# Kernel optimization log

Measured on AMD Instinct MI355X. Metric: run time of the kernel, lower is better.

## Reference

```python
import jax, jax.numpy as jnp
import numpy as np

N = 50000        # nodes
E = 800000       # edges (before self-loops)
F_IN = 128       # input features
HID = 32         # per-head hidden channels
H1 = 4           # heads of conv1
H2 = 8           # heads of conv2
NEG_SLOPE = 0.2  # PyG GATConv LeakyReLU slope
E_DEC = 100000   # pos/neg decode edges each


def setup_inputs() -> dict:
    key = jax.random.key(0)
    ks = jax.random.split(key, 12)
    s = 0.1
    return {
        "x": jax.random.normal(ks[0], (N, F_IN), jnp.float32),
        "edge_index": jax.random.randint(ks[1], (2, E), 0, N, dtype=jnp.int32),
        "pos_edge_index": jax.random.randint(ks[2], (2, E_DEC), 0, N, dtype=jnp.int32),
        "neg_edge_index": jax.random.randint(ks[3], (2, E_DEC), 0, N, dtype=jnp.int32),
        "W1": jax.random.normal(ks[4], (F_IN, H1 * HID), jnp.float32) * s,
        "a_src1": jax.random.normal(ks[5], (H1, HID), jnp.float32) * s,
        "a_dst1": jax.random.normal(ks[6], (H1, HID), jnp.float32) * s,
        "b1": jax.random.normal(ks[7], (H1 * HID,), jnp.float32) * s,
        "W2": jax.random.normal(ks[8], (H1 * HID, H2 * HID), jnp.float32) * s,
        "a_src2": jax.random.normal(ks[9], (H2, HID), jnp.float32) * s,
        "a_dst2": jax.random.normal(ks[10], (H2, HID), jnp.float32) * s,
        "b2": jax.random.normal(ks[11], (H2 * HID,), jnp.float32) * s,
    }


def _segment_softmax(e, seg, n):
    # softmax over edges grouped by destination node; max is detached (cancels analytically)
    m = jax.lax.stop_gradient(jax.ops.segment_max(e, seg, num_segments=n))
    ex = jnp.exp(e - m[seg])
    denom = jax.ops.segment_sum(ex, seg, num_segments=n)
    return ex / (denom[seg] + 1e-16)


def _gat_conv(x, src, dst, W, a_src, a_dst, b, heads, out_ch):
    n = x.shape[0]
    h = (x @ W).reshape(n, heads, out_ch)             # [N,H,C]
    al_s = (h * a_src[None]).sum(-1)                  # [N,H]
    al_d = (h * a_dst[None]).sum(-1)                  # [N,H]
    e = al_s[src] + al_d[dst]                         # [E,H] edge logits
    e = jnp.where(e > 0, e, NEG_SLOPE * e)            # LeakyReLU
    alpha = _segment_softmax(e, dst, n)               # [E,H]
    msg = h[src] * alpha[:, :, None]                  # [E,H,C]
    out = jax.ops.segment_sum(msg, dst, num_segments=n)  # [N,H,C]
    return out.reshape(n, heads * out_ch) + b


def reference(x, edge_index, pos_edge_index, neg_edge_index,
              W1, a_src1, a_dst1, b1, W2, a_src2, a_dst2, b2):
    n = x.shape[0]
    loops = jnp.arange(n, dtype=edge_index.dtype)     # PyG add_self_loops=True
    src = jnp.concatenate([edge_index[0], loops])
    dst = jnp.concatenate([edge_index[1], loops])
    # encode
    z = jax.nn.relu(_gat_conv(x, src, dst, W1, a_src1, a_dst1, b1, H1, HID))
    z = _gat_conv(z, src, dst, W2, a_src2, a_dst2, b2, H2, HID)
    # decode
    ei = jnp.concatenate([pos_edge_index, neg_edge_index], axis=1)
    logits = (z[ei[0]] * z[ei[1]]).sum(-1)            # [2*E_DEC]
    return logits
```

## Files before the change

### kernel.cpp

```cpp
#include <hip/hip_runtime.h>
#include <hip/hip_bf16.h>

#define NN 50000
#define EE 800000
#define ET (EE + NN)
#define F_IN 128
#define HID 32
#define H1 4
#define H2 8
#define E_DEC 100000
#define NEG_SLOPE 0.2f

typedef __attribute__((ext_vector_type(8))) short short8;
typedef __attribute__((ext_vector_type(4))) float floatx4;

__device__ __forceinline__ unsigned short f2b(float f) {
    __hip_bfloat16 h = __float2bfloat16(f);
    return *reinterpret_cast<unsigned short*>(&h);
}
__device__ __forceinline__ float b2f(unsigned short u) {
    return __uint_as_float(((unsigned int)u) << 16);
}

__device__ __forceinline__ void packW_one(const float* __restrict__ W,
                                          unsigned short* __restrict__ Wp, int OUT, int id) {
    const int ctg = id >> 8;
    const int ln = id & 63;
    const int col = ctg * 16 + (ln & 15);
    const int k0 = ((id >> 6) & 3) * 32 + ((ln >> 4) & 3) * 8;
    ushort4 lo, hi;
    lo.x = f2b(W[(k0 + 0) * OUT + col]);
    lo.y = f2b(W[(k0 + 1) * OUT + col]);
    lo.z = f2b(W[(k0 + 2) * OUT + col]);
    lo.w = f2b(W[(k0 + 3) * OUT + col]);
    hi.x = f2b(W[(k0 + 4) * OUT + col]);
    hi.y = f2b(W[(k0 + 5) * OUT + col]);
    hi.z = f2b(W[(k0 + 6) * OUT + col]);
    hi.w = f2b(W[(k0 + 7) * OUT + col]);
    ((ushort4*)Wp)[id * 2] = lo;
    ((ushort4*)Wp)[id * 2 + 1] = hi;
}

#define HIST_BLOCKS ((EE / 4 + 255) / 256)
#define PACK_BLOCKS ((6144 + 255) / 256)

__global__ void hist_pack_k(const int* __restrict__ ei, int* __restrict__ counts_p,
                            const int* __restrict__ probe, int* __restrict__ rank,
                            const float* __restrict__ W1, unsigned short* __restrict__ wp1,
                            const float* __restrict__ W2, unsigned short* __restrict__ wp2) {
    if (blockIdx.x < HIST_BLOCKS) {
        const int t = blockIdx.x * 256 + threadIdx.x;
        if (t >= EE / 4) return;
        const int pv = probe[0];
        int* cp = counts_p + (blockIdx.x & 7) * NN;
        const int4 d4 = ((const int4*)(ei + EE))[t];
        int4 r4;
        r4.x = atomicAdd(&cp[d4.x], 1) - pv;
        r4.y = atomicAdd(&cp[d4.y], 1) - pv;
        r4.z = atomicAdd(&cp[d4.z], 1) - pv;
        r4.w = atomicAdd(&cp[d4.w], 1) - pv;
        ((int4*)rank)[t] = r4;
    } else {
        const int id = (blockIdx.x - HIST_BLOCKS) * 256 + threadIdx.x;
        if (id < 2048) packW_one(W1, wp1, 128, id);
        else if (id < 6144) packW_one(W2, wp2, 256, id - 2048);
    }
}

__global__ void scan1_k(const int* __restrict__ counts_p, const int* __restrict__ probe,
                        int* __restrict__ bsum) {
    __shared__ int sh[256];
    const unsigned pv = (unsigned)probe[0];
    int t = threadIdx.x;
    int i = blockIdx.x * 256 + t;
    int deg = 0;
    if (i < NN) {
        unsigned sum = 0;
#pragma unroll
        for (int s = 0; s < 8; ++s) sum += (unsigned)counts_p[s * NN + i];
        deg = (int)(sum - 8u * pv) + 1;
    }
    sh[t] = deg;
    __syncthreads();
    for (int off = 128; off > 0; off >>= 1) {
        if (t < off) sh[t] += sh[t + off];
        __syncthreads();
    }
    if (t == 0) bsum[blockIdx.x] = sh[0];
}

__global__ void scan2_k(int* __restrict__ bsum, int nb, int* __restrict__ start) {
    __shared__ int sh[256];
    int t = threadIdx.x;
    int v = (t < nb) ? bsum[t] : 0;
    sh[t] = v;
    __syncthreads();
    for (int off = 1; off < 256; off <<= 1) {
        int u = (t >= off) ? sh[t - off] : 0;
        __syncthreads();
        sh[t] += u;
        __syncthreads();
    }
    if (t < nb) bsum[t] = sh[t] - v;
    if (t == 0) start[NN] = ET;
}

__global__ void scan3_k(const int* __restrict__ counts_p, const int* __restrict__ probe,
                        const int* __restrict__ bsum, int* __restrict__ start,
                        int* __restrict__ offs, int* __restrict__ csr) {
    __shared__ int sh[256];
    const unsigned pv = (unsigned)probe[0];
    int t = threadIdx.x;
    int i = blockIdx.x * 256 + t;
    int part[8];
    int deg = 0;
    if (i < NN) {
        deg = 1;
#pragma unroll
        for (int s = 0; s < 8; ++s) {
            part[s] = (int)((unsigned)counts_p[s * NN + i] - pv);
            deg += part[s];
        }
    }
    sh[t] = deg;
    __syncthreads();
    for (int off = 1; off < 256; off <<= 1) {
        int u = (t >= off) ? sh[t - off] : 0;
        __syncthreads();
        sh[t] += u;
        __syncthreads();
    }
    int excl = sh[t] - deg + bsum[blockIdx.x];
    if (i < NN) {
        start[i] = excl;
        int o = excl;
#pragma unroll
        for (int s = 0; s < 8; ++s) {
            offs[s * NN + i] = o;
            o += part[s];
        }
        csr[o] = i;
    }
}

__global__ void scatter_k(const int* __restrict__ ei, const int* __restrict__ rank,
                          const int* __restrict__ offs, int* __restrict__ csr) {
    const int t = blockIdx.x * 256 + threadIdx.x;
    if (t >= EE / 4) return;
    const int* off = offs + (blockIdx.x & 7) * NN;
    const int4 s4 = ((const int4*)ei)[t];
    const int4 d4 = ((const int4*)(ei + EE))[t];
    const int4 r4 = ((const int4*)rank)[t];
    csr[off[d4.x] + r4.x] = s4.x;
    csr[off[d4.y] + r4.y] = s4.y;
    csr[off[d4.z] + r4.z] = s4.z;
    csr[off[d4.w] + r4.w] = s4.w;
}

template <int OUT, int H, int CT, bool F32IN>
__global__ void gemm_k(const void* __restrict__ Xin, const unsigned short* __restrict__ Wp,
                       const float* __restrict__ a_src, const float* __restrict__ a_dst,
                       unsigned short* __restrict__ Hout, float* __restrict__ als,
                       float* __restrict__ ald) {
    const int wave = threadIdx.x >> 6;
    const int lane = threadIdx.x & 63;
    const int quad = lane >> 4;
    const int rl = lane & 15;
    const int r0 = blockIdx.x * 64;
    floatx4 acc[4][CT];
#pragma unroll
    for (int rt = 0; rt < 4; ++rt)
#pragma unroll
        for (int ct = 0; ct < CT; ++ct) acc[rt][ct] = {0.f, 0.f, 0.f, 0.f};

#pragma unroll
    for (int ks = 0; ks < 4; ++ks) {
        short8 a[4];
        const int c0k = ks * 32 + quad * 8;
#pragma unroll
        for (int rt = 0; rt < 4; ++rt) {
            int row = r0 + rt * 16 + rl;
            row = row < NN ? row : NN - 1;
            if (F32IN) {
                const float4* xp =
                    (const float4*)((const float*)Xin + (long long)row * 128 + c0k);
                const float4 v0 = xp[0];
                const float4 v1 = xp[1];
                short8 tt;
                tt[0] = (short)f2b(v0.x);
                tt[1] = (short)f2b(v0.y);
                tt[2] = (short)f2b(v0.z);
                tt[3] = (short)f2b(v0.w);
                tt[4] = (short)f2b(v1.x);
                tt[5] = (short)f2b(v1.y);
                tt[6] = (short)f2b(v1.z);
                tt[7] = (short)f2b(v1.w);
                a[rt] = tt;
            } else {
                a[rt] = *(const short8*)((const unsigned short*)Xin +
                                         (long long)row * 128 + c0k);
            }
        }
#pragma unroll
        for (int ct = 0; ct < CT; ++ct) {
            const int ctg = wave * CT + ct;
            const short8 b = *(const short8*)(Wp + (((ctg * 4 + ks) * 64 + lane) << 3));
#pragma unroll
            for (int rt = 0; rt < 4; ++rt)
                acc[rt][ct] = __builtin_amdgcn_mfma_f32_16x16x32_bf16(a[rt], b, acc[rt][ct], 0, 0, 0);
        }
    }
#pragma unroll
    for (int rt = 0; rt < 4; ++rt) {
        const int rowbase = r0 + rt * 16 + quad * 4;
#pragma unroll
        for (int ct = 0; ct < CT; ++ct) {
            const int col = (wave * CT + ct) * 16 + rl;
            unsigned short* hp = Hout + (long long)(col >> 5) * NN * 32 + (col & 31);
#pragma unroll
            for (int r = 0; r < 4; ++r) {
                const int row = rowbase + r;
                if (row < NN) hp[(long long)row * 32] = f2b(acc[rt][ct][r]);
            }
        }
    }
    float asv[CT], adv[CT];
#pragma unroll
    for (int ct = 0; ct < CT; ++ct) {
        const int col = (wave * CT + ct) * 16 + rl;
        asv[ct] = a_src[col];
        adv[ct] = a_dst[col];
    }
#pragma unroll
    for (int rt = 0; rt < 4; ++rt) {
#pragma unroll
        for (int r = 0; r < 4; ++r) {
            const int row = r0 + rt * 16 + quad * 4 + r;
            float ps[CT / 2], pd[CT / 2];
#pragma unroll
            for (int hh = 0; hh < CT / 2; ++hh) {
                ps[hh] = acc[rt][2 * hh][r] * asv[2 * hh] + acc[rt][2 * hh + 1][r] * asv[2 * hh + 1];
                pd[hh] = acc[rt][2 * hh][r] * adv[2 * hh] + acc[rt][2 * hh + 1][r] * adv[2 * hh + 1];
#pragma unroll
                for (int m = 8; m >= 1; m >>= 1) {
                    ps[hh] += __shfl_xor(ps[hh], m, 64);
                    pd[hh] += __shfl_xor(pd[hh], m, 64);
                }
            }
            if (rl == 0 && row < NN) {
#pragma unroll
                for (int hh = 0; hh < CT / 2; ++hh) {
                    const int hd = wave * (CT / 2) + hh;
                    als[(long long)hd * NN + row] = ps[hh];
                    ald[(long long)hd * NN + row] = pd[hh];
                }
            }
        }
    }
}

template <int OUT, int NSLICE, bool RELU>
__global__ void gathers_k(const int* __restrict__ start, const int* __restrict__ csr,
                          const float* __restrict__ als, const float* __restrict__ ald,
                          const unsigned short* __restrict__ Hin,
                          const float* __restrict__ bias, unsigned short* __restrict__ outp) {
    constexpr int SUB = 8 / NSLICE;
    const int xcd = blockIdx.x & 7;
    const int s = xcd / SUB;
    const int sub = xcd & (SUB - 1);
    const int wave = threadIdx.x >> 6;
    const int lane = threadIdx.x & 63;
    const int g = lane >> 3;
    const int cl = lane & 7;
    const int d = (blockIdx.x >> 3) * (32 * SUB) + sub * 32 + wave * 8 + g;
    if (d >= NN) return;
    const float* als_h = als + (long long)s * NN;
    const float aldd = ald[(long long)s * NN + d];
    const unsigned short* slab = Hin + (long long)s * NN * 32;
    const int beg = start[d], end = start[d + 1];
    float a0 = 0.f, a1 = 0.f, a2 = 0.f, a3 = 0.f, den = 0.f;
    int i = beg;
    for (; i + 7 < end; i += 8) {
        int sn[8];
        float l[8];
        ushort4 hv[8];
#pragma unroll
        for (int k = 0; k < 8; ++k) sn[k] = __builtin_nontemporal_load(csr + i + k);
#pragma unroll
        for (int k = 0; k < 8; ++k) l[k] = als_h[sn[k]] + aldd;
#pragma unroll
        for (int k = 0; k < 8; ++k) hv[k] = *(const ushort4*)(slab + (long long)sn[k] * 32 + cl * 4);
#pragma unroll
        for (int k = 0; k < 8; ++k) {
            float lg = l[k] > 0.f ? l[k] : NEG_SLOPE * l[k];
            const float w = __expf(lg);
            den += w;
            a0 += w * b2f(hv[k].x);
            a1 += w * b2f(hv[k].y);
            a2 += w * b2f(hv[k].z);
            a3 += w * b2f(hv[k].w);
        }
    }
    for (; i + 3 < end; i += 4) {
        int sn[4];
        float l[4];
        ushort4 hv[4];
#pragma unroll
        for (int k = 0; k < 4; ++k) sn[k] = __builtin_nontemporal_load(csr + i + k);
#pragma unroll
        for (int k = 0; k < 4; ++k) l[k] = als_h[sn[k]] + aldd;
#pragma unroll
        for (int k = 0; k < 4; ++k) hv[k] = *(const ushort4*)(slab + (long long)sn[k] * 32 + cl * 4);
#pragma unroll
        for (int k = 0; k < 4; ++k) {
            float lg = l[k] > 0.f ? l[k] : NEG_SLOPE * l[k];
            const float w = __expf(lg);
            den += w;
            a0 += w * b2f(hv[k].x);
            a1 += w * b2f(hv[k].y);
            a2 += w * b2f(hv[k].z);
            a3 += w * b2f(hv[k].w);
        }
    }
    for (; i < end; ++i) {
        const int sn = __builtin_nontemporal_load(csr + i);
        float lg = als_h[sn] + aldd;
        lg = lg > 0.f ? lg : NEG_SLOPE * lg;
        const float w = __expf(lg);
        const ushort4 hv = *(const ushort4*)(slab + (long long)sn * 32 + cl * 4);
        den += w;
        a0 += w * b2f(hv.x);
        a1 += w * b2f(hv.y);
        a2 += w * b2f(hv.z);
        a3 += w * b2f(hv.w);
    }
    const float inv = 1.f / (den + 1e-16f);
    const int c0 = s * 32 + cl * 4;
    float v0 = a0 * inv + bias[c0];
    float v1 = a1 * inv + bias[c0 + 1];
    float v2 = a2 * inv + bias[c0 + 2];
    float v3 = a3 * inv + bias[c0 + 3];
    if (RELU) {
        v0 = v0 > 0.f ? v0 : 0.f;
        v1 = v1 > 0.f ? v1 : 0.f;
        v2 = v2 > 0.f ? v2 : 0.f;
        v3 = v3 > 0.f ? v3 : 0.f;
    }
    unsigned long long pk =
        (unsigned long long)f2b(v0) |
        ((unsigned long long)f2b(v1) << 16) |
        ((unsigned long long)f2b(v2) << 32) |
        ((unsigned long long)f2b(v3) << 48);
    __builtin_nontemporal_store(pk, (unsigned long long*)(outp + (long long)d * OUT + c0));
}

__global__ void decode_s_k(const int* __restrict__ pei, const int* __restrict__ nei,
                           const unsigned short* __restrict__ z2, float* __restrict__ part) {
    const int s = blockIdx.x & 7;
    const int g = blockIdx.x >> 3;
    const int wave = threadIdx.x >> 6, lane = threadIdx.x & 63;
    const int slot = lane >> 3, cl = lane & 7;
    const int idx = g * 32 + wave * 8 + slot;
    if (idx >= 2 * E_DEC) return;
    int a, b;
    if (idx < E_DEC) {
        a = pei[idx];
        b = pei[E_DEC + idx];
    } else {
        const int j = idx - E_DEC;
        a = nei[j];
        b = nei[E_DEC + j];
    }
    const ushort4 ua = *(const ushort4*)(z2 + (long long)a * 256 + s * 32 + cl * 4);
    const ushort4 ub = *(const ushort4*)(z2 + (long long)b * 256 + s * 32 + cl * 4);
    float sum = b2f(ua.x) * b2f(ub.x) + b2f(ua.y) * b2f(ub.y) +
                b2f(ua.z) * b2f(ub.z) + b2f(ua.w) * b2f(ub.w);
    sum += __shfl_xor(sum, 4, 64);
    sum += __shfl_xor(sum, 2, 64);
    sum += __shfl_xor(sum, 1, 64);
    if (cl == 0) part[(long long)s * (2 * E_DEC) + idx] = sum;
}

__global__ void reduce_k(const float* __restrict__ part, float* __restrict__ out) {
    const int i = blockIdx.x * 256 + threadIdx.x;
    if (i >= 2 * E_DEC) return;
    float s = 0.f;
#pragma unroll
    for (int k = 0; k < 8; ++k) s += part[(long long)k * (2 * E_DEC) + i];
    out[i] = s;
}

extern "C" void kernel_launch(void* const* d_in, const int* in_sizes, int n_in,
                              void* d_out, int out_size, void* d_ws, size_t ws_size,
                              hipStream_t stream) {
    const float* x = (const float*)d_in[0];
    const int* ei = (const int*)d_in[1];
    const int* pei = (const int*)d_in[2];
    const int* nei = (const int*)d_in[3];
    const float* W1 = (const float*)d_in[4];
    const float* as1 = (const float*)d_in[5];
    const float* ad1 = (const float*)d_in[6];
    const float* b1 = (const float*)d_in[7];
    const float* W2 = (const float*)d_in[8];
    const float* as2 = (const float*)d_in[9];
    const float* ad2 = (const float*)d_in[10];
    const float* b2 = (const float*)d_in[11];
    float* out = (float*)d_out;

    unsigned short* h1 = (unsigned short*)d_ws;
    unsigned short* h2 = h1 + (long long)NN * 128;
    unsigned short* z2 = h2 + (long long)NN * 256;
    unsigned short* z1 = z2 + (long long)NN * 256;
    unsigned short* wp1 = z1 + (long long)NN * 128;
    unsigned short* wp2 = wp1 + 128 * 128;
    float* als1 = (float*)(wp2 + 128 * 256);
    float* ald1 = als1 + NN * H1;
    float* als2 = ald1 + NN * H1;
    float* ald2 = als2 + NN * H2;
    float* part = ald2 + NN * H2;
    int* counts_p = (int*)(part + 8 * 2 * E_DEC);
    int* start = counts_p + 8 * NN;
    int* offs = start + NN + 1;
    int* rank = offs + 8 * NN;
    int* bsum = rank + EE;
    int* csr = bsum + 256;
    int* probe = csr + ET;

    const int NB = (NN + 255) / 256;

    hist_pack_k<<<HIST_BLOCKS + PACK_BLOCKS, 256, 0, stream>>>(
        ei, counts_p, probe, rank, W1, wp1, W2, wp2);
    scan1_k<<<NB, 256, 0, stream>>>(counts_p, probe, bsum);
    scan2_k<<<1, 256, 0, stream>>>(bsum, NB, start);
    scan3_k<<<NB, 256, 0, stream>>>(counts_p, probe, bsum, start, offs, csr);
    scatter_k<<<HIST_BLOCKS, 256, 0, stream>>>(ei, rank, offs, csr);

    gemm_k<128, H1, 2, true><<<(NN + 63) / 64, 256, 0, stream>>>(
        x, wp1, as1, ad1, h1, als1, ald1);
    gathers_k<128, 4, true><<<8 * ((NN + 63) / 64), 256, 0, stream>>>(
        start, csr, als1, ald1, h1, b1, z1);

    gemm_k<256, H2, 4, false><<<(NN + 63) / 64, 256, 0, stream>>>(
        z1, wp2, as2, ad2, h2, als2, ald2);
    gathers_k<256, 8, false><<<8 * ((NN + 31) / 32), 256, 0, stream>>>(
        start, csr, als2, ald2, h2, b2, z2);

    decode_s_k<<<8 * ((2 * E_DEC + 31) / 32), 256, 0, stream>>>(pei, nei, z2, part);
    reduce_k<<<(2 * E_DEC + 255) / 256, 256, 0, stream>>>(part, out);
}
```

Measured before the change: 416.6 us.

## Sort destination nodes by degree to balance gather work across lanes

Builds a degree histogram during the CSR scan, prefix-sums it in scan2, and writes a degree-sorted node permutation in scan3. Both gather kernels then process nodes in that permuted order, so the 8 nodes sharing a wave have similar edge counts and less divergence in the per-node loops. The cost is extra global atomics on a 256-bin histogram and an indirection through perm. Output writes become scattered rather than contiguous. Index arithmetic also drops from 64-bit to 32-bit.

```diff
diff --git a/kernel.cpp b/kernel.cpp
--- a/kernel.cpp
+++ b/kernel.cpp
@@ -42,12 +42,13 @@
 }
 
 #define HIST_BLOCKS ((EE / 4 + 255) / 256)
-#define PACK_BLOCKS ((6144 + 255) / 256)
+#define PACK_BLOCKS 25
 
 __global__ void hist_pack_k(const int* __restrict__ ei, int* __restrict__ counts_p,
                             const int* __restrict__ probe, int* __restrict__ rank,
                             const float* __restrict__ W1, unsigned short* __restrict__ wp1,
-                            const float* __restrict__ W2, unsigned short* __restrict__ wp2) {
+                            const float* __restrict__ W2, unsigned short* __restrict__ wp2,
+                            int* __restrict__ dhist) {
     if (blockIdx.x < HIST_BLOCKS) {
         const int t = blockIdx.x * 256 + threadIdx.x;
         if (t >= EE / 4) return;
@@ -64,11 +65,12 @@
         const int id = (blockIdx.x - HIST_BLOCKS) * 256 + threadIdx.x;
         if (id < 2048) packW_one(W1, wp1, 128, id);
         else if (id < 6144) packW_one(W2, wp2, 256, id - 2048);
+        else if (id < 6400) dhist[id - 6144] = 0;
     }
 }
 
 __global__ void scan1_k(const int* __restrict__ counts_p, const int* __restrict__ probe,
-                        int* __restrict__ bsum) {
+                        int* __restrict__ bsum, int* __restrict__ dhist) {
     __shared__ int sh[256];
     const unsigned pv = (unsigned)probe[0];
     int t = threadIdx.x;
@@ -79,6 +81,7 @@
 #pragma unroll
         for (int s = 0; s < 8; ++s) sum += (unsigned)counts_p[s * NN + i];
         deg = (int)(sum - 8u * pv) + 1;
+        atomicAdd(&dhist[deg < 255 ? deg : 255], 1);
     }
     sh[t] = deg;
     __syncthreads();
@@ -89,7 +92,8 @@
     if (t == 0) bsum[blockIdx.x] = sh[0];
 }
 
-__global__ void scan2_k(int* __restrict__ bsum, int nb, int* __restrict__ start) {
+__global__ void scan2_k(int* __restrict__ bsum, int nb, int* __restrict__ start,
+                        int* __restrict__ dhist) {
     __shared__ int sh[256];
     int t = threadIdx.x;
     int v = (t < nb) ? bsum[t] : 0;
@@ -103,11 +107,23 @@
     }
     if (t < nb) bsum[t] = sh[t] - v;
     if (t == 0) start[NN] = ET;
+    __syncthreads();
+    int h = dhist[t];
+    sh[t] = h;
+    __syncthreads();
+    for (int off = 1; off < 256; off <<= 1) {
+        int u = (t >= off) ? sh[t - off] : 0;
+        __syncthreads();
+        sh[t] += u;
+        __syncthreads();
+    }
+    dhist[t] = sh[t] - h;
 }
 
 __global__ void scan3_k(const int* __restrict__ counts_p, const int* __restrict__ probe,
                         const int* __restrict__ bsum, int* __restrict__ start,
-                        int* __restrict__ offs, int* __restrict__ csr) {
+                        int* __restrict__ offs, int* __restrict__ csr,
+                        int* __restrict__ dhist, int* __restrict__ perm) {
     __shared__ int sh[256];
     const unsigned pv = (unsigned)probe[0];
     int t = threadIdx.x;
@@ -140,6 +156,9 @@
             o += part[s];
         }
         csr[o] = i;
+        const int bin = deg < 255 ? deg : 255;
+        const int pos = atomicAdd(&dhist[bin], 1);
+        perm[pos] = i;
     }
 }
 
@@ -261,6 +280,7 @@
 
 template <int OUT, int NSLICE, bool RELU>
 __global__ void gathers_k(const int* __restrict__ start, const int* __restrict__ csr,
+                          const int* __restrict__ perm,
                           const float* __restrict__ als, const float* __restrict__ ald,
                           const unsigned short* __restrict__ Hin,
                           const float* __restrict__ bias, unsigned short* __restrict__ outp) {
@@ -272,11 +292,12 @@
     const int lane = threadIdx.x & 63;
     const int g = lane >> 3;
     const int cl = lane & 7;
-    const int d = (blockIdx.x >> 3) * (32 * SUB) + sub * 32 + wave * 8 + g;
-    if (d >= NN) return;
-    const float* als_h = als + (long long)s * NN;
-    const float aldd = ald[(long long)s * NN + d];
-    const unsigned short* slab = Hin + (long long)s * NN * 32;
+    const int gidx = (blockIdx.x >> 3) * (32 * SUB) + sub * 32 + wave * 8 + g;
+    if (gidx >= NN) return;
+    const int d = perm[gidx];
+    const float* als_h = als + s * NN;
+    const float aldd = ald[s * NN + d];
+    const unsigned short* slab = Hin + s * (NN * 32);
     const int beg = start[d], end = start[d + 1];
     float a0 = 0.f, a1 = 0.f, a2 = 0.f, a3 = 0.f, den = 0.f;
     int i = beg;
@@ -289,7 +310,7 @@
 #pragma unroll
         for (int k = 0; k < 8; ++k) l[k] = als_h[sn[k]] + aldd;
 #pragma unroll
-        for (int k = 0; k < 8; ++k) hv[k] = *(const ushort4*)(slab + (long long)sn[k] * 32 + cl * 4);
+        for (int k = 0; k < 8; ++k) hv[k] = *(const ushort4*)(slab + sn[k] * 32 + cl * 4);
 #pragma unroll
         for (int k = 0; k < 8; ++k) {
             float lg = l[k] > 0.f ? l[k] : NEG_SLOPE * l[k];
@@ -310,7 +331,7 @@
 #pragma unroll
         for (int k = 0; k < 4; ++k) l[k] = als_h[sn[k]] + aldd;
 #pragma unroll
-        for (int k = 0; k < 4; ++k) hv[k] = *(const ushort4*)(slab + (long long)sn[k] * 32 + cl * 4);
+        for (int k = 0; k < 4; ++k) hv[k] = *(const ushort4*)(slab + sn[k] * 32 + cl * 4);
 #pragma unroll
         for (int k = 0; k < 4; ++k) {
             float lg = l[k] > 0.f ? l[k] : NEG_SLOPE * l[k];
@@ -327,7 +348,7 @@
         float lg = als_h[sn] + aldd;
         lg = lg > 0.f ? lg : NEG_SLOPE * lg;
         const float w = __expf(lg);
-        const ushort4 hv = *(const ushort4*)(slab + (long long)sn * 32 + cl * 4);
+        const ushort4 hv = *(const ushort4*)(slab + sn * 32 + cl * 4);
         den += w;
         a0 += w * b2f(hv.x);
         a1 += w * b2f(hv.y);
@@ -351,7 +372,7 @@
         ((unsigned long long)f2b(v1) << 16) |
         ((unsigned long long)f2b(v2) << 32) |
         ((unsigned long long)f2b(v3) << 48);
-    __builtin_nontemporal_store(pk, (unsigned long long*)(outp + (long long)d * OUT + c0));
+    __builtin_nontemporal_store(pk, (unsigned long long*)(outp + d * OUT + c0));
 }
 
 __global__ void decode_s_k(const int* __restrict__ pei, const int* __restrict__ nei,
@@ -424,26 +445,28 @@
     int* rank = offs + 8 * NN;
     int* bsum = rank + EE;
     int* csr = bsum + 256;
-    int* probe = csr + ET;
+    int* dhist = csr + ET;
+    int* perm = dhist + 256;
+    int* probe = perm + NN;
 
     const int NB = (NN + 255) / 256;
 
     hist_pack_k<<<HIST_BLOCKS + PACK_BLOCKS, 256, 0, stream>>>(
-        ei, counts_p, probe, rank, W1, wp1, W2, wp2);
-    scan1_k<<<NB, 256, 0, stream>>>(counts_p, probe, bsum);
-    scan2_k<<<1, 256, 0, stream>>>(bsum, NB, start);
-    scan3_k<<<NB, 256, 0, stream>>>(counts_p, probe, bsum, start, offs, csr);
+        ei, counts_p, probe, rank, W1, wp1, W2, wp2, dhist);
+    scan1_k<<<NB, 256, 0, stream>>>(counts_p, probe, bsum, dhist);
+    scan2_k<<<1, 256, 0, stream>>>(bsum, NB, start, dhist);
+    scan3_k<<<NB, 256, 0, stream>>>(counts_p, probe, bsum, start, offs, csr, dhist, perm);
     scatter_k<<<HIST_BLOCKS, 256, 0, stream>>>(ei, rank, offs, csr);
 
     gemm_k<128, H1, 2, true><<<(NN + 63) / 64, 256, 0, stream>>>(
         x, wp1, as1, ad1, h1, als1, ald1);
     gathers_k<128, 4, true><<<8 * ((NN + 63) / 64), 256, 0, stream>>>(
-        start, csr, als1, ald1, h1, b1, z1);
+        start, csr, perm, als1, ald1, h1, b1, z1);
 
     gemm_k<256, H2, 4, false><<<(NN + 63) / 64, 256, 0, stream>>>(
         z1, wp2, as2, ad2, h2, als2, ald2);
     gathers_k<256, 8, false><<<8 * ((NN + 31) / 32), 256, 0, stream>>>(
-        start, csr, als2, ald2, h2, b2, z2);
+        start, csr, perm, als2, ald2, h2, b2, z2);
 
     decode_s_k<<<8 * ((2 * E_DEC + 31) / 32), 256, 0, stream>>>(pei, nei, z2, part);
     reduce_k<<<(2 * E_DEC + 255) / 256, 256, 0, stream>>>(part, out);
```

Measured after the change: 726.2 us. 74.3% more time.
